# Kernel tuning notes

Hardware: AMD Instinct MI355X
Metric: run time of the kernel (lower is better)

## Reference

```python
import jax, jax.numpy as jnp
import numpy as np

E = 256      # embed_dim
K = 8        # kNN neighbors (hard-coded in module)
B = 64       # num cells (samples)
P = 512      # objects per cell (equal segments)
N = B * P
NUM_CLASSES = 31  # 30 known + <unk> (padding idx 0)


def _normalize(x, axis=-1):
    n = jnp.linalg.norm(x, axis=axis, keepdims=True)
    return x / jnp.clip(n, 1e-12, None)


def _mlp2(x, W1, b1, W2, b2):
    # get_mlp([d_in, 64/E, d_out]): Linear-ReLU-Linear
    return jax.nn.relu(x @ W1 + b1) @ W2 + b2


def setup_inputs() -> dict:
    key = jax.random.key(0)
    ks = jax.random.split(key, 32)

    def w(k, shape, s=0.05):
        return (jax.random.normal(k, shape, jnp.float32) * s).astype(jnp.float32)

    class_table = w(ks[0], (NUM_CLASSES, E))
    class_table = class_table.at[0].set(0.0)  # padding_idx=0

    inp = {
        # learned params
        "class_table": class_table,
        "colorW1": w(ks[1], (3, 64)), "colorb1": jnp.zeros((64,), jnp.float32),
        "colorW2": w(ks[2], (64, E)), "colorb2": jnp.zeros((E,), jnp.float32),
        "posW1": w(ks[3], (3, 64)), "posb1": jnp.zeros((64,), jnp.float32),
        "posW2": w(ks[4], (64, E)), "posb2": jnp.zeros((E,), jnp.float32),
        "mergeW": w(ks[5], (3 * E, E)), "mergeb": jnp.zeros((E,), jnp.float32),
        # DynamicEdgeConv mlp: Linear(2E,E)-ReLU-BN(E)-Linear(E,E)
        "gW1": w(ks[6], (2 * E, E)), "gb1": jnp.zeros((E,), jnp.float32),
        "g_gamma": jnp.ones((E,), jnp.float32), "g_beta": jnp.zeros((E,), jnp.float32),
        "gW2": w(ks[7], (E, E)), "gb2": jnp.zeros((E,), jnp.float32),
        # final lin: Linear(E,E)-ReLU-Linear(E,E)
        "lW1": w(ks[8], (E, E)), "lb1": jnp.zeros((E,), jnp.float32),
        "lW2": w(ks[9], (E, E)), "lb2": jnp.zeros((E,), jnp.float32),
        # forward inputs
        "positions": jax.random.normal(ks[10], (N, 3), jnp.float32),
        "colors": jax.random.uniform(ks[11], (N, 3), jnp.float32),
        "class_indices": jax.random.randint(ks[12], (N,), 0, NUM_CLASSES, jnp.int64),
        "num_samples": B,
    }
    return inp


def reference(class_table, colorW1, colorb1, colorW2, colorb2,
              posW1, posb1, posW2, posb2, mergeW, mergeb,
              gW1, gb1, g_gamma, g_beta, gW2, gb2,
              lW1, lb1, lW2, lb2,
              positions, colors, class_indices, num_samples):
    # --- per-object embeddings, each L2-normalized, then merged ---
    ce = _normalize(class_table[class_indices])                         # [N,E]
    co = _normalize(_mlp2(colors, colorW1, colorb1, colorW2, colorb2))  # [N,E]
    pe = _normalize(_mlp2(positions, posW1, posb1, posW2, posb2))       # [N,E]
    emb = jnp.concatenate([ce, co, pe], axis=-1) @ mergeW + mergeb      # [N,E]

    # --- DynamicEdgeConv (variation 0): per-sample kNN in feature space ---
    x = emb.reshape(num_samples, -1, E)                                 # [B,P,E]
    sq = jnp.sum(x * x, axis=-1)                                        # [B,P]
    dist = sq[:, :, None] + sq[:, None, :] - 2.0 * jnp.einsum('bpe,bqe->bpq', x, x)
    _, idx = jax.lax.top_k(-dist, K)                                    # [B,P,K] (incl. self)

    x_nb = jax.vmap(lambda xb, ib: xb[ib])(x, idx)                      # [B,P,K,E]
    x_i = jnp.broadcast_to(x[:, :, None, :], x_nb.shape)
    msg_in = jnp.concatenate([x_i, x_nb - x_i], axis=-1)                # [B,P,K,2E]
    h = jax.nn.relu(msg_in @ gW1 + gb1)
    h = h * g_gamma + g_beta          # BatchNorm1d eval mode (running mean 0, var 1)
    h = h @ gW2 + gb2                                                   # [B,P,K,E]
    x1 = jnp.max(h, axis=2)                                             # max aggr -> [B,P,E]

    # --- global max pool over objects, final MLP, L2 normalize ---
    pooled = jnp.max(x1, axis=1)                                        # [B,E]
    out = _mlp2(pooled, lW1, lb1, lW2, lb2)
    return _normalize(out, axis=-1)
```

## Files before the change

kernel.cpp:

```cpp
#include <hip/hip_runtime.h>

#define EDIM 256
#define KNN 8
#define NB 64
#define NP 512
#define NTOT (NB * NP)

typedef short s16x8 __attribute__((ext_vector_type(8)));
typedef float f32x4 __attribute__((ext_vector_type(4)));
typedef float f32x16 __attribute__((ext_vector_type(16)));
typedef unsigned short ushort;

__device__ __forceinline__ ushort f2b(float f) {
    unsigned u = __float_as_uint(f);
    u = (u + 0x7fffu + ((u >> 16) & 1u)) >> 16;
    return (ushort)u;
}
__device__ __forceinline__ float b2f(ushort h) {
    return __uint_as_float(((unsigned)h) << 16);
}
__device__ __forceinline__ void split2(float x, ushort& h, ushort& l) {
    h = f2b(x);
    l = f2b(x - b2f(h));
}
__device__ __forceinline__ ushort f2bt(float f) {
    return (ushort)(__float_as_uint(f) >> 16);
}
__device__ __forceinline__ void split2t(float x, ushort& h, ushort& l) {
    h = f2bt(x);
    l = f2bt(x - b2f(h));
}

__device__ __forceinline__ void gload16(const ushort* g, ushort* l) {
    __builtin_amdgcn_global_load_lds(
        (const __attribute__((address_space(1))) void*)g,
        (__attribute__((address_space(3))) void*)l, 16, 0, 0);
}

__global__ __launch_bounds__(256)
void k_cvt(const float* __restrict__ gW1, const float* __restrict__ gW2,
           const float* __restrict__ g_gamma, const float* __restrict__ g_beta,
           const float* __restrict__ gb2,
           const float* __restrict__ cW2, const float* __restrict__ pW2,
           ushort* __restrict__ Wdh, ushort* __restrict__ Wdl,
           ushort* __restrict__ Wbh, ushort* __restrict__ Wbl,
           ushort* __restrict__ g2h, ushort* __restrict__ g2l,
           float* __restrict__ hb,
           ushort* __restrict__ cW2Th, ushort* __restrict__ cW2Tl,
           ushort* __restrict__ pW2Th, ushort* __restrict__ pW2Tl)
{
    const int gid = blockIdx.x * 256 + threadIdx.x;
    ushort h, l;
    if (gid < 65536) {
        const int n = gid >> 8, k = gid & 255;
        split2(gW1[k * 256 + n] - gW1[(k + 256) * 256 + n], h, l);
        Wdh[gid] = h; Wdl[gid] = l;
    } else if (gid < 131072) {
        const int i = gid - 65536, n = i >> 8, k = i & 255;
        split2(gW1[(k + 256) * 256 + n], h, l);
        Wbh[i] = h; Wbl[i] = l;
    } else if (gid < 196608) {
        const int i = gid - 131072, n = i >> 8, k = i & 255;
        split2(g_gamma[k] * gW2[k * 256 + n], h, l);
        g2h[i] = h; g2l[i] = l;
    } else if (gid < 196864) {
        const int n = gid - 196608;
        float s = gb2[n];
        for (int k = 0; k < 256; ++k) s += g_beta[k] * gW2[k * 256 + n];
        hb[n] = s;
    } else if (gid < 213248) {
        const int i = gid - 196864, n = i >> 6, k = i & 63;
        split2(cW2[k * 256 + n], h, l);
        cW2Th[i] = h; cW2Tl[i] = l;
    } else if (gid < 229632) {
        const int i = gid - 213248, n = i >> 6, k = i & 63;
        split2(pW2[k * 256 + n], h, l);
        pW2Th[i] = h; pW2Tl[i] = l;
    }
}

__global__ __launch_bounds__(256)
void k_fold(const float* __restrict__ cW2, const float* __restrict__ pW2,
            const float* __restrict__ cb2, const float* __restrict__ pb2,
            const float* __restrict__ mW,
            ushort* __restrict__ WcTh, ushort* __restrict__ WcTl,
            ushort* __restrict__ WpTh, ushort* __restrict__ WpTl,
            float* __restrict__ cbM, float* __restrict__ pbM)
{
    const int gid = blockIdx.x * 256 + threadIdx.x;
    ushort h, l;
    if (gid < 16384) {
        const int j = gid >> 8, n = gid & 255;
        float s = 0.f;
        for (int k = 0; k < 256; ++k) s += cW2[j * 256 + k] * mW[(256 + k) * 256 + n];
        split2(s, h, l);
        WcTh[n * 64 + j] = h; WcTl[n * 64 + j] = l;
    } else if (gid < 32768) {
        const int i = gid - 16384, j = i >> 8, n = i & 255;
        float s = 0.f;
        for (int k = 0; k < 256; ++k) s += pW2[j * 256 + k] * mW[(512 + k) * 256 + n];
        split2(s, h, l);
        WpTh[n * 64 + j] = h; WpTl[n * 64 + j] = l;
    } else if (gid < 33024) {
        const int n = gid - 32768;
        float s = 0.f;
        for (int k = 0; k < 256; ++k) s += cb2[k] * mW[(256 + k) * 256 + n];
        cbM[n] = s;
    } else if (gid < 33280) {
        const int n = gid - 33024;
        float s = 0.f;
        for (int k = 0; k < 256; ++k) s += pb2[k] * mW[(512 + k) * 256 + n];
        pbM[n] = s;
    }
}

__global__ __launch_bounds__(256)
void k_cls(const float* __restrict__ ct, const float* __restrict__ mW,
           float* __restrict__ classMn)
{
    __shared__ float ctn[256];
    __shared__ float red[4];
    const int c = blockIdx.x, t = threadIdx.x;
    const float v = ct[c * 256 + t];
    float ss = v * v;
    #pragma unroll
    for (int s = 32; s > 0; s >>= 1) ss += __shfl_down(ss, s, 64);
    if ((t & 63) == 0) red[t >> 6] = ss;
    __syncthreads();
    const float tot = red[0] + red[1] + red[2] + red[3];
    const float r = 1.f / fmaxf(sqrtf(tot), 1e-12f);
    ctn[t] = v * r;
    __syncthreads();
    float s = 0.f;
    for (int k = 0; k < 256; ++k) s += ctn[k] * mW[k * 256 + t];
    classMn[c * 256 + t] = s;
}

__global__ __launch_bounds__(256)
void k_embed(const float* __restrict__ classMn,
             const float* __restrict__ cW1, const float* __restrict__ cb1,
             const float* __restrict__ cb2,
             const float* __restrict__ pW1, const float* __restrict__ pb1,
             const float* __restrict__ pb2,
             const float* __restrict__ mb,
             const ushort* __restrict__ cW2Th, const ushort* __restrict__ cW2Tl,
             const ushort* __restrict__ pW2Th, const ushort* __restrict__ pW2Tl,
             const ushort* __restrict__ WcTh, const ushort* __restrict__ WcTl,
             const ushort* __restrict__ WpTh, const ushort* __restrict__ WpTl,
             const float* __restrict__ cbM, const float* __restrict__ pbM,
             const float* __restrict__ positions, const float* __restrict__ colors,
             const int* __restrict__ cls, const int cstride,
             ushort* __restrict__ ehi, ushort* __restrict__ elo,
             float* __restrict__ sqn)
{
    __shared__ __align__(16) ushort Ahc[16 * 72];
    __shared__ __align__(16) ushort Alc[16 * 72];
    __shared__ __align__(16) ushort Ahp[16 * 72];
    __shared__ __align__(16) ushort Alp[16 * 72];
    __shared__ float sqc[16][4], sqp_[16][4], sqe[16][4];

    const int t = threadIdx.x, w = t >> 6, lane = t & 63;
    const int l15 = lane & 15, quad = lane >> 4;
    const int obase = blockIdx.x * 16;

    {
        const int o = lane >> 4;
        const int objl = w * 4 + o;
        const int gobj = obase + objl;
        const float c0 = colors[gobj * 3], c1 = colors[gobj * 3 + 1], c2 = colors[gobj * 3 + 2];
        const float q0 = positions[gobj * 3], q1 = positions[gobj * 3 + 1], q2 = positions[gobj * 3 + 2];
        const int u0 = (lane & 15) * 4;
        #pragma unroll
        for (int uu = 0; uu < 4; ++uu) {
            const int u = u0 + uu;
            const float hc = fmaxf(cb1[u] + c0 * cW1[u] + c1 * cW1[64 + u] + c2 * cW1[128 + u], 0.f);
            const float hp = fmaxf(pb1[u] + q0 * pW1[u] + q1 * pW1[64 + u] + q2 * pW1[128 + u], 0.f);
            ushort h, l;
            split2(hc, h, l); Ahc[objl * 72 + u] = h; Alc[objl * 72 + u] = l;
            split2(hp, h, l); Ahp[objl * 72 + u] = h; Alp[objl * 72 + u] = l;
        }
    }
    __syncthreads();

    f32x4 aco[4], ape[4];
    #pragma unroll
    for (int nt = 0; nt < 4; ++nt) { aco[nt] = (f32x4){0.f,0.f,0.f,0.f}; ape[nt] = (f32x4){0.f,0.f,0.f,0.f}; }

    #pragma unroll
    for (int kt = 0; kt < 2; ++kt) {
        const int ao = l15 * 72 + kt * 32 + quad * 8;
        const s16x8 ahc = *(const s16x8*)&Ahc[ao];
        const s16x8 alc = *(const s16x8*)&Alc[ao];
        const s16x8 ahp = *(const s16x8*)&Ahp[ao];
        const s16x8 alp = *(const s16x8*)&Alp[ao];
        #pragma unroll
        for (int nt = 0; nt < 4; ++nt) {
            const int n = w * 64 + nt * 16 + l15;
            const size_t bo = (size_t)n * 64 + kt * 32 + quad * 8;
            const s16x8 cbh = *(const s16x8*)(cW2Th + bo);
            const s16x8 cbl = *(const s16x8*)(cW2Tl + bo);
            const s16x8 pbh = *(const s16x8*)(pW2Th + bo);
            const s16x8 pbl = *(const s16x8*)(pW2Tl + bo);
            aco[nt] = __builtin_amdgcn_mfma_f32_16x16x32_bf16(ahc, cbh, aco[nt], 0, 0, 0);
            ape[nt] = __builtin_amdgcn_mfma_f32_16x16x32_bf16(ahp, pbh, ape[nt], 0, 0, 0);
            aco[nt] = __builtin_amdgcn_mfma_f32_16x16x32_bf16(alc, cbh, aco[nt], 0, 0, 0);
            ape[nt] = __builtin_amdgcn_mfma_f32_16x16x32_bf16(alp, pbh, ape[nt], 0, 0, 0);
            aco[nt] = __builtin_amdgcn_mfma_f32_16x16x32_bf16(ahc, cbl, aco[nt], 0, 0, 0);
            ape[nt] = __builtin_amdgcn_mfma_f32_16x16x32_bf16(ahp, pbl, ape[nt], 0, 0, 0);
        }
    }

    float sc[4] = {0.f,0.f,0.f,0.f}, sp[4] = {0.f,0.f,0.f,0.f};
    #pragma unroll
    for (int nt = 0; nt < 4; ++nt) {
        const int col = w * 64 + nt * 16 + l15;
        const float cbv = cb2[col], pbv = pb2[col];
        #pragma unroll
        for (int r = 0; r < 4; ++r) {
            const float co = aco[nt][r] + cbv;
            const float pe = ape[nt][r] + pbv;
            sc[r] += co * co;
            sp[r] += pe * pe;
        }
    }
    #pragma unroll
    for (int s = 8; s > 0; s >>= 1) {
        #pragma unroll
        for (int r = 0; r < 4; ++r) {
            sc[r] += __shfl_xor(sc[r], s, 64);
            sp[r] += __shfl_xor(sp[r], s, 64);
        }
    }
    if (l15 == 0) {
        #pragma unroll
        for (int r = 0; r < 4; ++r) { sqc[quad * 4 + r][w] = sc[r]; sqp_[quad * 4 + r][w] = sp[r]; }
    }
    __syncthreads();

    float rco[4], rpe[4];
    #pragma unroll
    for (int r = 0; r < 4; ++r) {
        const int row = quad * 4 + r;
        rco[r] = 1.f / fmaxf(sqrtf(sqc[row][0] + sqc[row][1] + sqc[row][2] + sqc[row][3]), 1e-12f);
        rpe[r] = 1.f / fmaxf(sqrtf(sqp_[row][0] + sqp_[row][1] + sqp_[row][2] + sqp_[row][3]), 1e-12f);
    }

    f32x4 ac[4], ap[4];
    #pragma unroll
    for (int nt = 0; nt < 4; ++nt) { ac[nt] = (f32x4){0.f,0.f,0.f,0.f}; ap[nt] = (f32x4){0.f,0.f,0.f,0.f}; }

    #pragma unroll
    for (int kt = 0; kt < 2; ++kt) {
        const int ao = l15 * 72 + kt * 32 + quad * 8;
        const s16x8 ahc = *(const s16x8*)&Ahc[ao];
        const s16x8 alc = *(const s16x8*)&Alc[ao];
        const s16x8 ahp = *(const s16x8*)&Ahp[ao];
        const s16x8 alp = *(const s16x8*)&Alp[ao];
        #pragma unroll
        for (int nt = 0; nt < 4; ++nt) {
            const int n = w * 64 + nt * 16 + l15;
            const size_t bo = (size_t)n * 64 + kt * 32 + quad * 8;
            const s16x8 cbh = *(const s16x8*)(WcTh + bo);
            const s16x8 cbl = *(const s16x8*)(WcTl + bo);
            const s16x8 pbh = *(const s16x8*)(WpTh + bo);
            const s16x8 pbl = *(const s16x8*)(WpTl + bo);
            ac[nt] = __builtin_amdgcn_mfma_f32_16x16x32_bf16(ahc, cbh, ac[nt], 0, 0, 0);
            ap[nt] = __builtin_amdgcn_mfma_f32_16x16x32_bf16(ahp, pbh, ap[nt], 0, 0, 0);
            ac[nt] = __builtin_amdgcn_mfma_f32_16x16x32_bf16(alc, cbh, ac[nt], 0, 0, 0);
            ap[nt] = __builtin_amdgcn_mfma_f32_16x16x32_bf16(alp, pbh, ap[nt], 0, 0, 0);
            ac[nt] = __builtin_amdgcn_mfma_f32_16x16x32_bf16(ahc, cbl, ac[nt], 0, 0, 0);
            ap[nt] = __builtin_amdgcn_mfma_f32_16x16x32_bf16(ahp, pbl, ap[nt], 0, 0, 0);
        }
    }

    int ci[4];
    #pragma unroll
    for (int r = 0; r < 4; ++r) {
        const int gobj = obase + quad * 4 + r;
        int c = cls[(size_t)gobj * cstride];
        if ((unsigned)c > 30u) c = 0;
        ci[r] = c;
    }

    float rp[4] = {0.f,0.f,0.f,0.f};
    #pragma unroll
    for (int nt = 0; nt < 4; ++nt) {
        const int col = w * 64 + nt * 16 + l15;
        const float mbv = mb[col], cbMv = cbM[col], pbMv = pbM[col];
        #pragma unroll
        for (int r = 0; r < 4; ++r) {
            const int row = quad * 4 + r;
            const float e = classMn[ci[r] * 256 + col]
                          + rco[r] * (ac[nt][r] + cbMv)
                          + rpe[r] * (ap[nt][r] + pbMv) + mbv;
            ushort h, l;
            split2(e, h, l);
            ehi[(size_t)(obase + row) * 256 + col] = h;
            elo[(size_t)(obase + row) * 256 + col] = l;
            rp[r] += e * e;
        }
    }
    #pragma unroll
    for (int s = 8; s > 0; s >>= 1) {
        #pragma unroll
        for (int r = 0; r < 4; ++r) rp[r] += __shfl_xor(rp[r], s, 64);
    }
    if (l15 == 0) {
        #pragma unroll
        for (int r = 0; r < 4; ++r) sqe[quad * 4 + r][w] = rp[r];
    }
    __syncthreads();
    if (t < 16) sqn[obase + t] = sqe[t][0] + sqe[t][1] + sqe[t][2] + sqe[t][3];
}

__global__ __launch_bounds__(256)
void k_gram(const ushort* __restrict__ ehi, const ushort* __restrict__ elo,
            const float* __restrict__ sqn, float* __restrict__ dist)
{
    __shared__ __align__(16) ushort lds[2][4][4096];

    const int t = threadIdx.x, w = t >> 6, lane = t & 63;
    const int l15 = lane & 15, quad = lane >> 4;
    const int b = blockIdx.x;
    const int xcd = b & 7, rest = b >> 3;
    const int cell = xcd * 8 + (rest >> 4);
    const int tile = rest & 15;
    const int p0 = (tile >> 2) * 128, q0 = (tile & 3) * 128;
    const size_t cb = (size_t)cell * NP;
    const int diag = (p0 == q0);
    const int wr = w >> 1, wc = w & 1;

    int srow[2], scol[2];
    #pragma unroll
    for (int i = 0; i < 2; ++i) {
        const int p = (w * 2 + i) * 64 + lane;
        const int row = p >> 2;
        srow[i] = row;
        scol[i] = ((p & 3) ^ ((row >> 1) & 3)) * 8;
    }

    #define STAGE(KT, D)                                                         \
    {                                                                            \
        const int kb_ = (KT) * 32;                                               \
        _Pragma("unroll")                                                        \
        for (int i = 0; i < 2; ++i) {                                            \
            const int ls_ = (w * 2 + i) * 512;               \
            const size_t ga_ = (cb + p0 + srow[i]) * 256 + kb_ + scol[i];        \
            gload16(ehi + ga_, &lds[D][0][ls_]);                                 \
            gload16(elo + ga_, &lds[D][1][ls_]);                                 \
            if (!diag) {                                                         \
                const size_t gq_ = (cb + q0 + srow[i]) * 256 + kb_ + scol[i];    \
                gload16(ehi + gq_, &lds[D][2][ls_]);                             \
                gload16(elo + gq_, &lds[D][3][ls_]);                             \
            }                                                                    \
        }                                                                        \
    }

    f32x4 acc[4][4];
    #pragma unroll
    for (int mt = 0; mt < 4; ++mt)
        #pragma unroll
        for (int nt = 0; nt < 4; ++nt) acc[mt][nt] = (f32x4){0.f, 0.f, 0.f, 0.f};

    const int bB = diag ? 0 : 2;

    STAGE(0, 0);
    __syncthreads();

    for (int kt = 0; kt < 8; ++kt) {
        const int cur = kt & 1;
        if (kt < 7) STAGE(kt + 1, cur ^ 1);

        s16x8 ah[4], al[4];
        #pragma unroll
        for (int mt = 0; mt < 4; ++mt) {
            const int r = wr * 64 + mt * 16 + l15;
            const int slot = 4 * r + (quad ^ ((r >> 1) & 3));
            ah[mt] = *(const s16x8*)&lds[cur][0][slot * 8];
            al[mt] = *(const s16x8*)&lds[cur][1][slot * 8];
        }
        #pragma unroll
        for (int nt = 0; nt < 4; ++nt) {
            const int rq = wc * 64 + nt * 16 + l15;
            const int slot = 4 * rq + (quad ^ ((rq >> 1) & 3));
            const s16x8 bh = *(const s16x8*)&lds[cur][bB][slot * 8];
            const s16x8 bl = *(const s16x8*)&lds[cur][bB + 1][slot * 8];
            #pragma unroll
            for (int mt = 0; mt < 4; ++mt) {
                acc[mt][nt] = __builtin_amdgcn_mfma_f32_16x16x32_bf16(ah[mt], bh, acc[mt][nt], 0, 0, 0);
                acc[mt][nt] = __builtin_amdgcn_mfma_f32_16x16x32_bf16(al[mt], bh, acc[mt][nt], 0, 0, 0);
                acc[mt][nt] = __builtin_amdgcn_mfma_f32_16x16x32_bf16(ah[mt], bl, acc[mt][nt], 0, 0, 0);
            }
        }
        __syncthreads();
    }
    #undef STAGE

    float sqp[4][4];
    #pragma unroll
    for (int mt = 0; mt < 4; ++mt)
        #pragma unroll
        for (int r = 0; r < 4; ++r)
            sqp[mt][r] = sqn[cb + p0 + wr * 64 + mt * 16 + quad * 4 + r];

    #pragma unroll
    for (int nt = 0; nt < 4; ++nt) {
        const int colq = q0 + wc * 64 + nt * 16 + l15;
        const float sq_q = sqn[cb + colq];
        #pragma unroll
        for (int mt = 0; mt < 4; ++mt) {
            #pragma unroll
            for (int r = 0; r < 4; ++r) {
                const int rowp = p0 + wr * 64 + mt * 16 + quad * 4 + r;
                __builtin_nontemporal_store((sqp[mt][r] + sq_q) - 2.f * acc[mt][nt][r],
                                            &dist[(cb + rowp) * NP + colq]);
            }
        }
    }
}

__global__ __launch_bounds__(256)
void k_select(const float* __restrict__ dist, int* __restrict__ nidx)
{
    const int wv = threadIdx.x >> 6, lane = threadIdx.x & 63;
    const int xcd = blockIdx.x & 7, rest = blockIdx.x >> 3;
    const int cell = xcd * 8 + (rest >> 7);
    const int p = cell * NP + (rest & 127) * 4 + wv;
    const float* row = dist + (size_t)p * NP;

    float d[8];
    {
        const float4 va = *(const float4*)(row + lane * 8);
        const float4 vb = *(const float4*)(row + lane * 8 + 4);
        d[0] = va.x; d[1] = va.y; d[2] = va.z; d[3] = va.w;
        d[4] = vb.x; d[5] = vb.y; d[6] = vb.z; d[7] = vb.w;
    }

    for (int r = 0; r < KNN; ++r) {
        float bd = d[0]; int bi = 0;
        #pragma unroll
        for (int i = 1; i < 8; ++i)
            if (d[i] < bd) { bd = d[i]; bi = i; }
        int bq = lane * 8 + bi;
        #pragma unroll
        for (int s = 32; s > 0; s >>= 1) {
            const float od = __shfl_down(bd, s, 64);
            const int oq = __shfl_down(bq, s, 64);
            if (od < bd || (od == bd && oq < bq)) { bd = od; bq = oq; }
        }
        const int win = __shfl(bq, 0, 64);
        if (lane == 0) nidx[(size_t)p * KNN + r] = ((p >> 9) << 9) | win;
        if ((win >> 3) == lane) {
            const int wi = win & 7;
            #pragma unroll
            for (int i = 0; i < 8; ++i) if (wi == i) d[i] = 3.4e38f;
        }
    }
}

__global__ __launch_bounds__(256)
void k_uv(const ushort* __restrict__ ehi, const ushort* __restrict__ elo,
          const ushort* __restrict__ Wdh, const ushort* __restrict__ Wbh,
          const float* __restrict__ gb1,
          float* __restrict__ u, float* __restrict__ v)
{
    (void)elo;
    __shared__ __align__(16) ushort lds[2][2048];

    const int t = threadIdx.x, w = t >> 6, lane = t & 63;
    const int l15 = lane & 15, quad = lane >> 4;
    const int isV = blockIdx.x >> 9;
    const int m0 = (blockIdx.x & 511) * 64;
    const ushort* Wh = isV ? Wbh : Wdh;
    float* out = isV ? v : u;
    const int mh = w & 1, ch = w >> 1;

    const int sp = w * 64 + lane;
    const int srow = sp >> 2;
    const int scol = ((sp & 3) ^ ((srow >> 1) & 3)) * 8;

    #define STAGE_UV(S, D)                                                       \
    {                                                                            \
        const size_t ga_ = (size_t)(m0 + srow) * 256 + (S) * 32 + scol;          \
        gload16(ehi + ga_, &lds[D][sp * 8]);                                     \
    }

    const int r0 = mh * 32 + l15, r1 = r0 + 16;
    const int slot0 = 4 * r0 + (quad ^ ((r0 >> 1) & 3));
    const int slot1 = 4 * r1 + (quad ^ ((r1 >> 1) & 3));

    f32x4 acc[2][8];
    #pragma unroll
    for (int mt = 0; mt < 2; ++mt)
        #pragma unroll
        for (int nt = 0; nt < 8; ++nt) acc[mt][nt] = (f32x4){0.f, 0.f, 0.f, 0.f};

    STAGE_UV(0, 0);
    __syncthreads();

    for (int s = 0; s < 8; ++s) {
        const int cur = s & 1;
        if (s < 7) STAGE_UV(s + 1, cur ^ 1);

        const s16x8 ah0 = *(const s16x8*)&lds[cur][slot0 * 8];
        const s16x8 ah1 = *(const s16x8*)&lds[cur][slot1 * 8];
        #pragma unroll
        for (int nt = 0; nt < 8; ++nt) {
            const int n = ch * 128 + nt * 16 + l15;
            const size_t bo = (size_t)n * 256 + s * 32 + quad * 8;
            const s16x8 bh = *(const s16x8*)(Wh + bo);
            acc[0][nt] = __builtin_amdgcn_mfma_f32_16x16x32_bf16(ah0, bh, acc[0][nt], 0, 0, 0);
            acc[1][nt] = __builtin_amdgcn_mfma_f32_16x16x32_bf16(ah1, bh, acc[1][nt], 0, 0, 0);
        }
        __syncthreads();
    }
    #undef STAGE_UV

    #pragma unroll
    for (int mt = 0; mt < 2; ++mt) {
        #pragma unroll
        for (int nt = 0; nt < 8; ++nt) {
            const int col = ch * 128 + nt * 16 + l15;
            const float bias = isV ? 0.f : gb1[col];
            #pragma unroll
            for (int r = 0; r < 4; ++r) {
                const int row = mh * 32 + mt * 16 + quad * 4 + r;
                out[(size_t)(m0 + row) * 256 + col] = acc[mt][nt][r] + bias;
            }
        }
    }
}

__global__ __launch_bounds__(512)
void k_edge(const float* __restrict__ u, const float* __restrict__ v,
            const int* __restrict__ nidx,
            const ushort* __restrict__ g2h,
            const float* __restrict__ hb,
            float* __restrict__ part)
{
    __shared__ ushort Abuf[2][2304];
    __shared__ float ustage[2048];

    const int t = threadIdx.x, w = t >> 6, lane = t & 63;
    const int l31 = lane & 31, kh = lane >> 5;

    const int b = blockIdx.x;
    const int xcd = b & 7, rest = b >> 3;
    const int cell = xcd * 8 + (rest >> 6);
    const int pl0 = cell * NP + (rest & 63) * 8;

    {
        const int pt = t >> 6, kk = (t & 63) * 4;
        *(float4*)&ustage[pt * 256 + kk] = *(const float4*)(u + (size_t)(pl0 + pt) * 256 + kk);
    }

    const int se = t >> 3, kq = t & 7;
    const int upt = se >> 3;
    int svrow = nidx[(size_t)(pl0 + upt) * KNN + (se & 7)];
    if ((unsigned)svrow >= (unsigned)NTOT) svrow = 0;

    __syncthreads();

    float4 vr[2];

    #define VLOAD(S)                                                             \
    {                                                                            \
        const int k0 = (S) * 32 + kq * 4;                                        \
        vr[(S) & 1] = *(const float4*)(v + (size_t)svrow * 256 + k0);            \
    }
    #define SPLITW(S, BUF)                                                       \
    {                                                                            \
        const int k0u = (S) * 32 + kq * 4;                                       \
        const float4 ua = *(const float4*)&ustage[upt * 256 + k0u];              \
        const float4 va = vr[(S) & 1];                                           \
        const float sv[4] = {                                                    \
            fmaxf(ua.x + va.x, 0.f), fmaxf(ua.y + va.y, 0.f),                    \
            fmaxf(ua.z + va.z, 0.f), fmaxf(ua.w + va.w, 0.f)};                   \
        union { uint2 q; ushort us[4]; } th;                                     \
        _Pragma("unroll")                                                        \
        for (int j = 0; j < 4; ++j) { th.us[j] = f2b(sv[j]); }                   \
        *(uint2*)&Abuf[BUF][se * 36 + kq * 4] = th.q;                            \
    }

    #define LDS_BARRIER()                                                        \
    {                                                                            \
        asm volatile("s_waitcnt lgkmcnt(0)" ::: "memory");                       \
        __builtin_amdgcn_s_barrier();                                            \
    }

    f32x16 acc[2];
    acc[0] = (f32x16)(0.0f);
    acc[1] = (f32x16)(0.0f);

    VLOAD(0); VLOAD(1);
    SPLITW(0, 0);

    #pragma unroll
    for (int s = 0; s < 8; ++s) {
        LDS_BARRIER();
        if (s < 7) {
            SPLITW(s + 1, (s + 1) & 1);
            if (s < 6) VLOAD(s + 2);
        }

        s16x8 ah[2][2];
        #pragma unroll
        for (int mt = 0; mt < 2; ++mt) {
            #pragma unroll
            for (int kc = 0; kc < 2; ++kc) {
                const int ao = (mt * 32 + l31) * 36 + kc * 16 + kh * 8;
                union { uint2 q[2]; s16x8 v8; } Th;
                Th.q[0] = *(const uint2*)&Abuf[s & 1][ao];
                Th.q[1] = *(const uint2*)&Abuf[s & 1][ao + 4];
                ah[mt][kc] = Th.v8;
            }
        }

        #pragma unroll
        for (int kc = 0; kc < 2; ++kc) {
            const int n = w * 32 + l31;
            const s16x8 bh = *(const s16x8*)(g2h + (size_t)n * 256 + s * 32 + kc * 16 + kh * 8);
            acc[0] = __builtin_amdgcn_mfma_f32_32x32x16_bf16(ah[0][kc], bh, acc[0], 0, 0, 0);
            acc[1] = __builtin_amdgcn_mfma_f32_32x32x16_bf16(ah[1][kc], bh, acc[1], 0, 0, 0);
        }
    }
    #undef VLOAD
    #undef SPLITW
    #undef LDS_BARRIER

    const int slot = rest & 63;
    {
        float rm = -3.4e38f;
        #pragma unroll
        for (int r = 0; r < 16; ++r)
            rm = fmaxf(rm, fmaxf(acc[0][r], acc[1][r]));
        rm = fmaxf(rm, __shfl_xor(rm, 32, 64));
        if (kh == 0) {
            const int col = w * 32 + l31;
            part[((size_t)cell * 64 + slot) * 256 + col] = rm + hb[col];
        }
    }
}

__global__ __launch_bounds__(256)
void k_final(const float* __restrict__ part,
             const float* __restrict__ lW1, const float* __restrict__ lb1,
             const float* __restrict__ lW2, const float* __restrict__ lb2,
             float* __restrict__ out)
{
    __shared__ float pooled[256];
    __shared__ float hid[256];
    __shared__ float red[4];

    const int b = blockIdx.x;
    const int t = threadIdx.x;

    float m = -3.4e38f;
    for (int s = 0; s < 64; ++s)
        m = fmaxf(m, part[((size_t)b * 64 + s) * 256 + t]);
    pooled[t] = m;
    __syncthreads();

    float h = lb1[t];
    for (int k = 0; k < 256; k += 4) {
        #pragma unroll
        for (int kk = 0; kk < 4; ++kk)
            h += pooled[k + kk] * lW1[(k + kk) * 256 + t];
    }
    hid[t] = fmaxf(h, 0.f);
    __syncthreads();

    float o = lb2[t];
    for (int k = 0; k < 256; k += 4) {
        #pragma unroll
        for (int kk = 0; kk < 4; ++kk)
            o += hid[k + kk] * lW2[(k + kk) * 256 + t];
    }

    float ss = o * o;
    #pragma unroll
    for (int s = 32; s > 0; s >>= 1) ss += __shfl_down(ss, s, 64);
    if ((t & 63) == 0) red[t >> 6] = ss;
    __syncthreads();
    const float tot = red[0] + red[1] + red[2] + red[3];
    const float rn = 1.f / fmaxf(sqrtf(tot), 1e-12f);
    out[b * 256 + t] = o * rn;
}

extern "C" void kernel_launch(void* const* d_in, const int* in_sizes, int n_in,
                              void* d_out, int out_size, void* d_ws, size_t ws_size,
                              hipStream_t stream)
{
    (void)n_in; (void)out_size; (void)ws_size;

    const float* class_table = (const float*)d_in[0];
    const float* cW1 = (const float*)d_in[1];
    const float* cb1 = (const float*)d_in[2];
    const float* cW2 = (const float*)d_in[3];
    const float* cb2 = (const float*)d_in[4];
    const float* pW1 = (const float*)d_in[5];
    const float* pb1 = (const float*)d_in[6];
    const float* pW2 = (const float*)d_in[7];
    const float* pb2 = (const float*)d_in[8];
    const float* mW  = (const float*)d_in[9];
    const float* mb  = (const float*)d_in[10];
    const float* gW1 = (const float*)d_in[11];
    const float* gb1 = (const float*)d_in[12];
    const float* g_gamma = (const float*)d_in[13];
    const float* g_beta  = (const float*)d_in[14];
    const float* gW2 = (const float*)d_in[15];
    const float* gb2 = (const float*)d_in[16];
    const float* lW1 = (const float*)d_in[17];
    const float* lb1 = (const float*)d_in[18];
    const float* lW2 = (const float*)d_in[19];
    const float* lb2 = (const float*)d_in[20];
    const float* positions = (const float*)d_in[21];
    const float* colors    = (const float*)d_in[22];
    const int*  cls        = (const int*)d_in[23];

    const int cstride = (in_sizes[23] == 2 * NTOT) ? 2 : 1;

    char* base = (char*)d_ws;
    float*   part   = (float*)(base + 0);
    ushort*  Wdh    = (ushort*)(base + 4194304);
    ushort*  Wdl    = (ushort*)(base + 4325376);
    ushort*  Wbh    = (ushort*)(base + 4456448);
    ushort*  Wbl    = (ushort*)(base + 4587520);
    ushort*  g2h    = (ushort*)(base + 4718592);
    ushort*  g2l    = (ushort*)(base + 4849664);
    float*   hb     = (float*)(base + 4980736);
    ushort*  cW2Th  = (ushort*)(base + 4981760);
    ushort*  cW2Tl  = (ushort*)(base + 5014528);
    ushort*  pW2Th  = (ushort*)(base + 5047296);
    ushort*  pW2Tl  = (ushort*)(base + 5080064);
    ushort*  WcTh   = (ushort*)(base + 5112832);
    ushort*  WcTl   = (ushort*)(base + 5145600);
    ushort*  WpTh   = (ushort*)(base + 5178368);
    ushort*  WpTl   = (ushort*)(base + 5211136);
    float*   classMn= (float*)(base + 5243904);
    float*   cbM    = (float*)(base + 5275648);
    float*   pbM    = (float*)(base + 5276672);
    int*     nidx   = (int*)(base + 5277696);
    float*   sqn    = (float*)(base + 6326272);
    ushort*  ehi    = (ushort*)(base + 6457344);
    ushort*  elo    = (ushort*)(base + 23234560);
    float*   dist   = (float*)(base + 40011776);
    float*   v      = (float*)(base + 107120640);
    float*   u      = (float*)(base + 140675072);
    float* out = (float*)d_out;

    k_cvt<<<897, 256, 0, stream>>>(gW1, gW2, g_gamma, g_beta, gb2, cW2, pW2,
                                   Wdh, Wdl, Wbh, Wbl, g2h, g2l, hb,
                                   cW2Th, cW2Tl, pW2Th, pW2Tl);
    k_fold<<<130, 256, 0, stream>>>(cW2, pW2, cb2, pb2, mW,
                                    WcTh, WcTl, WpTh, WpTl, cbM, pbM);
    k_cls<<<31, 256, 0, stream>>>(class_table, mW, classMn);

    k_embed<<<NTOT / 16, 256, 0, stream>>>(classMn, cW1, cb1, cb2, pW1, pb1, pb2,
                                           mb, cW2Th, cW2Tl, pW2Th, pW2Tl,
                                           WcTh, WcTl, WpTh, WpTl, cbM, pbM,
                                           positions, colors, cls, cstride,
                                           ehi, elo, sqn);
    k_gram<<<NB * 16, 256, 0, stream>>>(ehi, elo, sqn, dist);
    k_select<<<NTOT / 4, 256, 0, stream>>>(dist, nidx);
    k_uv<<<2 * NTOT / 64, 256, 0, stream>>>(ehi, elo, Wdh, Wbh, gb1, u, v);
    k_edge<<<NTOT / 8, 512, 0, stream>>>(u, v, nidx, g2h, hb, part);
    k_final<<<NB, 256, 0, stream>>>(part, lW1, lb1, lW2, lb2, out);
}
```

Before: 417.4 us.

## Exploit Gram symmetry: compute upper-triangle tiles and mirror via LDS transpose; merge prep kernels

The pairwise-distance kernel now computes only the 10 upper-triangular 128x128 tiles per cell instead of all 16. Each off-diagonal tile is also written transposed to the mirrored location, staged through swizzled LDS so the global stores stay coalesced. This removes about 37% of the Gram MFMA work and the matching operand loads, at the cost of extra LDS traffic and a barrier in the epilogue. Separately, the three weight-prep kernels are merged into one launch to cut launch overhead. One risk: the symmetric mirror may differ bitwise from a directly computed value, which could change tie-breaking in top-k.

```diff
diff --git a/kernel.cpp b/kernel.cpp
--- a/kernel.cpp
+++ b/kernel.cpp
@@ -23,13 +23,6 @@
     h = f2b(x);
     l = f2b(x - b2f(h));
 }
-__device__ __forceinline__ ushort f2bt(float f) {
-    return (ushort)(__float_as_uint(f) >> 16);
-}
-__device__ __forceinline__ void split2t(float x, ushort& h, ushort& l) {
-    h = f2bt(x);
-    l = f2bt(x - b2f(h));
-}
 
 __device__ __forceinline__ void gload16(const ushort* g, ushort* l) {
     __builtin_amdgcn_global_load_lds(
@@ -38,102 +31,101 @@
 }
 
 __global__ __launch_bounds__(256)
-void k_cvt(const float* __restrict__ gW1, const float* __restrict__ gW2,
-           const float* __restrict__ g_gamma, const float* __restrict__ g_beta,
-           const float* __restrict__ gb2,
-           const float* __restrict__ cW2, const float* __restrict__ pW2,
-           ushort* __restrict__ Wdh, ushort* __restrict__ Wdl,
-           ushort* __restrict__ Wbh, ushort* __restrict__ Wbl,
-           ushort* __restrict__ g2h, ushort* __restrict__ g2l,
-           float* __restrict__ hb,
-           ushort* __restrict__ cW2Th, ushort* __restrict__ cW2Tl,
-           ushort* __restrict__ pW2Th, ushort* __restrict__ pW2Tl)
-{
-    const int gid = blockIdx.x * 256 + threadIdx.x;
-    ushort h, l;
-    if (gid < 65536) {
-        const int n = gid >> 8, k = gid & 255;
-        split2(gW1[k * 256 + n] - gW1[(k + 256) * 256 + n], h, l);
-        Wdh[gid] = h; Wdl[gid] = l;
-    } else if (gid < 131072) {
-        const int i = gid - 65536, n = i >> 8, k = i & 255;
-        split2(gW1[(k + 256) * 256 + n], h, l);
-        Wbh[i] = h; Wbl[i] = l;
-    } else if (gid < 196608) {
-        const int i = gid - 131072, n = i >> 8, k = i & 255;
-        split2(g_gamma[k] * gW2[k * 256 + n], h, l);
-        g2h[i] = h; g2l[i] = l;
-    } else if (gid < 196864) {
-        const int n = gid - 196608;
-        float s = gb2[n];
-        for (int k = 0; k < 256; ++k) s += g_beta[k] * gW2[k * 256 + n];
-        hb[n] = s;
-    } else if (gid < 213248) {
-        const int i = gid - 196864, n = i >> 6, k = i & 63;
-        split2(cW2[k * 256 + n], h, l);
-        cW2Th[i] = h; cW2Tl[i] = l;
-    } else if (gid < 229632) {
-        const int i = gid - 213248, n = i >> 6, k = i & 63;
-        split2(pW2[k * 256 + n], h, l);
-        pW2Th[i] = h; pW2Tl[i] = l;
-    }
-}
-
-__global__ __launch_bounds__(256)
-void k_fold(const float* __restrict__ cW2, const float* __restrict__ pW2,
+void k_prep(const float* __restrict__ gW1, const float* __restrict__ gW2,
+            const float* __restrict__ g_gamma, const float* __restrict__ g_beta,
+            const float* __restrict__ gb2,
+            const float* __restrict__ cW2, const float* __restrict__ pW2,
             const float* __restrict__ cb2, const float* __restrict__ pb2,
-            const float* __restrict__ mW,
+            const float* __restrict__ mW, const float* __restrict__ ct,
+            ushort* __restrict__ Wdh, ushort* __restrict__ Wdl,
+            ushort* __restrict__ Wbh, ushort* __restrict__ Wbl,
+            ushort* __restrict__ g2h, ushort* __restrict__ g2l,
+            float* __restrict__ hb,
+            ushort* __restrict__ cW2Th, ushort* __restrict__ cW2Tl,
+            ushort* __restrict__ pW2Th, ushort* __restrict__ pW2Tl,
             ushort* __restrict__ WcTh, ushort* __restrict__ WcTl,
             ushort* __restrict__ WpTh, ushort* __restrict__ WpTl,
-            float* __restrict__ cbM, float* __restrict__ pbM)
-{
-    const int gid = blockIdx.x * 256 + threadIdx.x;
-    ushort h, l;
-    if (gid < 16384) {
-        const int j = gid >> 8, n = gid & 255;
-        float s = 0.f;
-        for (int k = 0; k < 256; ++k) s += cW2[j * 256 + k] * mW[(256 + k) * 256 + n];
-        split2(s, h, l);
-        WcTh[n * 64 + j] = h; WcTl[n * 64 + j] = l;
-    } else if (gid < 32768) {
-        const int i = gid - 16384, j = i >> 8, n = i & 255;
-        float s = 0.f;
-        for (int k = 0; k < 256; ++k) s += pW2[j * 256 + k] * mW[(512 + k) * 256 + n];
-        split2(s, h, l);
-        WpTh[n * 64 + j] = h; WpTl[n * 64 + j] = l;
-    } else if (gid < 33024) {
-        const int n = gid - 32768;
-        float s = 0.f;
-        for (int k = 0; k < 256; ++k) s += cb2[k] * mW[(256 + k) * 256 + n];
-        cbM[n] = s;
-    } else if (gid < 33280) {
-        const int n = gid - 33024;
-        float s = 0.f;
-        for (int k = 0; k < 256; ++k) s += pb2[k] * mW[(512 + k) * 256 + n];
-        pbM[n] = s;
-    }
-}
-
-__global__ __launch_bounds__(256)
-void k_cls(const float* __restrict__ ct, const float* __restrict__ mW,
-           float* __restrict__ classMn)
+            float* __restrict__ cbM, float* __restrict__ pbM,
+            float* __restrict__ classMn)
 {
     __shared__ float ctn[256];
     __shared__ float red[4];
-    const int c = blockIdx.x, t = threadIdx.x;
-    const float v = ct[c * 256 + t];
-    float ss = v * v;
-    #pragma unroll
-    for (int s = 32; s > 0; s >>= 1) ss += __shfl_down(ss, s, 64);
-    if ((t & 63) == 0) red[t >> 6] = ss;
-    __syncthreads();
-    const float tot = red[0] + red[1] + red[2] + red[3];
-    const float r = 1.f / fmaxf(sqrtf(tot), 1e-12f);
-    ctn[t] = v * r;
-    __syncthreads();
-    float s = 0.f;
-    for (int k = 0; k < 256; ++k) s += ctn[k] * mW[k * 256 + t];
-    classMn[c * 256 + t] = s;
+    const int bid = blockIdx.x, t = threadIdx.x;
+    ushort h, l;
+
+    if (bid < 897) {
+        const int gid = bid * 256 + t;
+        if (gid < 65536) {
+            const int n = gid >> 8, k = gid & 255;
+            split2(gW1[k * 256 + n] - gW1[(k + 256) * 256 + n], h, l);
+            Wdh[gid] = h; Wdl[gid] = l;
+        } else if (gid < 131072) {
+            const int i = gid - 65536, n = i >> 8, k = i & 255;
+            split2(gW1[(k + 256) * 256 + n], h, l);
+            Wbh[i] = h; Wbl[i] = l;
+        } else if (gid < 196608) {
+            const int i = gid - 131072, n = i >> 8, k = i & 255;
+            split2(g_gamma[k] * gW2[k * 256 + n], h, l);
+            g2h[i] = h; g2l[i] = l;
+        } else if (gid < 196864) {
+            const int n = gid - 196608;
+            float s = gb2[n];
+            for (int k = 0; k < 256; ++k) s += g_beta[k] * gW2[k * 256 + n];
+            hb[n] = s;
+        } else if (gid < 213248) {
+            const int i = gid - 196864, n = i >> 6, k = i & 63;
+            split2(cW2[k * 256 + n], h, l);
+            cW2Th[i] = h; cW2Tl[i] = l;
+        } else if (gid < 229632) {
+            const int i = gid - 213248, n = i >> 6, k = i & 63;
+            split2(pW2[k * 256 + n], h, l);
+            pW2Th[i] = h; pW2Tl[i] = l;
+        }
+        return;
+    }
+    if (bid < 1027) {
+        const int gid = (bid - 897) * 256 + t;
+        if (gid < 16384) {
+            const int j = gid >> 8, n = gid & 255;
+            float s = 0.f;
+            for (int k = 0; k < 256; ++k) s += cW2[j * 256 + k] * mW[(256 + k) * 256 + n];
+            split2(s, h, l);
+            WcTh[n * 64 + j] = h; WcTl[n * 64 + j] = l;
+        } else if (gid < 32768) {
+            const int i = gid - 16384, j = i >> 8, n = i & 255;
+            float s = 0.f;
+            for (int k = 0; k < 256; ++k) s += pW2[j * 256 + k] * mW[(512 + k) * 256 + n];
+            split2(s, h, l);
+            WpTh[n * 64 + j] = h; WpTl[n * 64 + j] = l;
+        } else if (gid < 33024) {
+            const int n = gid - 32768;
+            float s = 0.f;
+            for (int k = 0; k < 256; ++k) s += cb2[k] * mW[(256 + k) * 256 + n];
+            cbM[n] = s;
+        } else if (gid < 33280) {
+            const int n = gid - 33024;
+            float s = 0.f;
+            for (int k = 0; k < 256; ++k) s += pb2[k] * mW[(512 + k) * 256 + n];
+            pbM[n] = s;
+        }
+        return;
+    }
+    {
+        const int c = bid - 1027;
+        const float v = ct[c * 256 + t];
+        float ss = v * v;
+        #pragma unroll
+        for (int s = 32; s > 0; s >>= 1) ss += __shfl_down(ss, s, 64);
+        if ((t & 63) == 0) red[t >> 6] = ss;
+        __syncthreads();
+        const float tot = red[0] + red[1] + red[2] + red[3];
+        const float r = 1.f / fmaxf(sqrtf(tot), 1e-12f);
+        ctn[t] = v * r;
+        __syncthreads();
+        float s = 0.f;
+        for (int k = 0; k < 256; ++k) s += ctn[k] * mW[k * 256 + t];
+        classMn[c * 256 + t] = s;
+    }
 }
 
 __global__ __launch_bounds__(256)
@@ -323,11 +315,14 @@
     const int l15 = lane & 15, quad = lane >> 4;
     const int b = blockIdx.x;
     const int xcd = b & 7, rest = b >> 3;
-    const int cell = xcd * 8 + (rest >> 4);
-    const int tile = rest & 15;
-    const int p0 = (tile >> 2) * 128, q0 = (tile & 3) * 128;
+    const int cell = xcd * 8 + rest / 10;
+    const int tt = rest % 10;
+    const int ti = (tt < 4) ? 0 : (tt < 7) ? 1 : (tt < 9) ? 2 : 3;
+    const int tbase = (ti == 0) ? 0 : (ti == 1) ? 4 : (ti == 2) ? 7 : 9;
+    const int tj = ti + (tt - tbase);
+    const int p0 = ti * 128, q0 = tj * 128;
     const size_t cb = (size_t)cell * NP;
-    const int diag = (p0 == q0);
+    const int diag = (ti == tj);
     const int wr = w >> 1, wc = w & 1;
 
     int srow[2], scol[2];
@@ -403,18 +398,34 @@
         for (int r = 0; r < 4; ++r)
             sqp[mt][r] = sqn[cb + p0 + wr * 64 + mt * 16 + quad * 4 + r];
 
+    float* T = (float*)&lds[0][0][0];
+
     #pragma unroll
     for (int nt = 0; nt < 4; ++nt) {
-        const int colq = q0 + wc * 64 + nt * 16 + l15;
+        const int cq_l = wc * 64 + nt * 16 + l15;
+        const int colq = q0 + cq_l;
         const float sq_q = sqn[cb + colq];
         #pragma unroll
         for (int mt = 0; mt < 4; ++mt) {
             #pragma unroll
             for (int r = 0; r < 4; ++r) {
-                const int rowp = p0 + wr * 64 + mt * 16 + quad * 4 + r;
-                __builtin_nontemporal_store((sqp[mt][r] + sq_q) - 2.f * acc[mt][nt][r],
-                                            &dist[(cb + rowp) * NP + colq]);
+                const int rp_l = wr * 64 + mt * 16 + quad * 4 + r;
+                const float d = (sqp[mt][r] + sq_q) - 2.f * acc[mt][nt][r];
+                __builtin_nontemporal_store(d, &dist[(cb + p0 + rp_l) * NP + colq]);
+                if (!diag) T[cq_l * 128 + (rp_l ^ ((cq_l & 7) << 4))] = d;
             }
+        }
+    }
+
+    if (!diag) {
+        __syncthreads();
+        const int l31 = t & 31, rbase = t >> 5;
+        #pragma unroll
+        for (int i = 0; i < 16; ++i) {
+            const int row = rbase + i * 8;
+            const int p4 = l31 * 4;
+            const f32x4 vv = *(const f32x4*)&T[row * 128 + (p4 ^ ((row & 7) << 4))];
+            __builtin_nontemporal_store(vv, (f32x4*)&dist[(cb + q0 + row) * NP + p0 + p4]);
         }
     }
 }
@@ -749,19 +760,18 @@
     float*   u      = (float*)(base + 140675072);
     float* out = (float*)d_out;
 
-    k_cvt<<<897, 256, 0, stream>>>(gW1, gW2, g_gamma, g_beta, gb2, cW2, pW2,
-                                   Wdh, Wdl, Wbh, Wbl, g2h, g2l, hb,
-                                   cW2Th, cW2Tl, pW2Th, pW2Tl);
-    k_fold<<<130, 256, 0, stream>>>(cW2, pW2, cb2, pb2, mW,
-                                    WcTh, WcTl, WpTh, WpTl, cbM, pbM);
-    k_cls<<<31, 256, 0, stream>>>(class_table, mW, classMn);
+    k_prep<<<1058, 256, 0, stream>>>(gW1, gW2, g_gamma, g_beta, gb2, cW2, pW2,
+                                     cb2, pb2, mW, class_table,
+                                     Wdh, Wdl, Wbh, Wbl, g2h, g2l, hb,
+                                     cW2Th, cW2Tl, pW2Th, pW2Tl,
+                                     WcTh, WcTl, WpTh, WpTl, cbM, pbM, classMn);
 
     k_embed<<<NTOT / 16, 256, 0, stream>>>(classMn, cW1, cb1, cb2, pW1, pb1, pb2,
                                            mb, cW2Th, cW2Tl, pW2Th, pW2Tl,
                                            WcTh, WcTl, WpTh, WpTl, cbM, pbM,
                                            positions, colors, cls, cstride,
                                            ehi, elo, sqn);
-    k_gram<<<NB * 16, 256, 0, stream>>>(ehi, elo, sqn, dist);
+    k_gram<<<NB * 10, 256, 0, stream>>>(ehi, elo, sqn, dist);
     k_select<<<NTOT / 4, 256, 0, stream>>>(dist, nidx);
     k_uv<<<2 * NTOT / 64, 256, 0, stream>>>(ehi, elo, Wdh, Wbh, gb1, u, v);
     k_edge<<<NTOT / 8, 512, 0, stream>>>(u, v, nidx, g2h, hb, part);
```

Result: faster. 404.9 us (-3.0%).
